# Performance work log

Hardware: AMD Instinct MI355X
Metric: run time of the kernel (lower is better)

## Reference

```python
import jax, jax.numpy as jnp
import numpy as np

B, S, D, H, FF = 2, 4096, 1024, 16, 4096
HD = D // H


def _layernorm(x, g, b, eps=1e-5):
    mu = jnp.mean(x, axis=-1, keepdims=True)
    var = jnp.var(x, axis=-1, keepdims=True)
    return (x - mu) * jax.lax.rsqrt(var + eps) * g + b


def setup_inputs() -> dict:
    key = jax.random.key(0)
    ks = jax.random.split(key, 20)
    sd = 1.0 / np.sqrt(D)
    sf = 1.0 / np.sqrt(FF)
    inp = {
        "x": jax.random.normal(ks[0], (B, S, D), jnp.float32),
        # attention projections, stored as [in, out]
        "wq": jax.random.normal(ks[1], (D, D), jnp.float32) * sd,
        "bq": jnp.zeros((D,), jnp.float32),
        "wk": jax.random.normal(ks[2], (D, D), jnp.float32) * sd,
        "bk": jnp.zeros((D,), jnp.float32),
        "wv": jax.random.normal(ks[3], (D, D), jnp.float32) * sd,
        "bv": jnp.zeros((D,), jnp.float32),
        "wo": jax.random.normal(ks[4], (D, D), jnp.float32) * sd,
        "bo": jnp.zeros((D,), jnp.float32),
        # block norm1 (pre-attention)
        "ln1_g": jnp.ones((D,), jnp.float32),
        "ln1_b": jnp.zeros((D,), jnp.float32),
        # FFN internal norm
        "lnf_g": jnp.ones((D,), jnp.float32),
        "lnf_b": jnp.zeros((D,), jnp.float32),
        # gated FFN
        "w1": jax.random.normal(ks[5], (D, FF), jnp.float32) * sd,
        "b1": jnp.zeros((FF,), jnp.float32),
        "wg": jax.random.normal(ks[6], (D, FF), jnp.float32) * sd,
        "bg": jnp.zeros((FF,), jnp.float32),
        "w2": jax.random.normal(ks[7], (FF, D), jnp.float32) * sf,
        "b2": jnp.zeros((D,), jnp.float32),
    }
    return inp


def reference(x, wq, bq, wk, bk, wv, bv, wo, bo, ln1_g, ln1_b,
              lnf_g, lnf_b, w1, b1, wg, bg, w2, b2):
    # pre-norm attention
    residual = x
    h = _layernorm(x, ln1_g, ln1_b)
    q = (h @ wq + bq).reshape(B, S, H, HD).transpose(0, 2, 1, 3)  # [B,H,S,hd]
    k = (h @ wk + bk).reshape(B, S, H, HD).transpose(0, 2, 1, 3)
    v = (h @ wv + bv).reshape(B, S, H, HD).transpose(0, 2, 1, 3)
    scores = jnp.einsum("bhqd,bhkd->bhqk", q, k) / np.sqrt(HD)
    attn = jax.nn.softmax(scores, axis=-1)  # [B,H,S,S] materialized as in torch src
    ctx = jnp.einsum("bhqk,bhkd->bhqd", attn, v)
    ctx = ctx.transpose(0, 2, 1, 3).reshape(B, S, D)
    attn_out = ctx @ wo + bo
    x = residual + attn_out  # dropout = 0 (eval)

    # gated FFN with internal pre-norm and residual
    res2 = x
    h2 = _layernorm(x, lnf_g, lnf_b)
    gate = jax.nn.sigmoid(h2 @ wg + bg)
    up = jax.nn.gelu(h2 @ w1 + b1, approximate=False)
    out = (up * gate) @ w2 + b2
    return out + res2
```

## Files before the change

kernel.cpp:

```cpp
#include <hip/hip_runtime.h>
#include <hip/hip_bf16.h>

#define BB 2
#define SS 4096
#define DD 1024
#define HH 16
#define HD 64
#define FF 4096
#define MM (BB*SS)
#define QKVW 3072

typedef __hip_bfloat16 bf16;
typedef __attribute__((ext_vector_type(8))) __bf16 v8bf;
typedef __attribute__((ext_vector_type(4))) float f32x4;
typedef __attribute__((ext_vector_type(16))) float f32x16;
typedef __attribute__((ext_vector_type(8))) unsigned short u16v8;

__device__ __forceinline__ f32x4 mfma16(v8bf a, v8bf b, f32x4 c) {
  return __builtin_amdgcn_mfma_f32_16x16x32_bf16(a, b, c, 0, 0, 0);
}
__device__ __forceinline__ f32x16 mfma32(v8bf a, v8bf b, f32x16 c) {
  return __builtin_amdgcn_mfma_f32_32x32x16_bf16(a, b, c, 0, 0, 0);
}
__device__ __forceinline__ void gload16(const void* g, void* l) {
  __builtin_amdgcn_global_load_lds((const __attribute__((address_space(1))) void*)g,
                                   (__attribute__((address_space(3))) void*)l, 16, 0, 0);
}
__device__ __forceinline__ unsigned cvtpk_bf16(float lo, float hi) {
  unsigned r;
  asm("v_cvt_pk_bf16_f32 %0, %1, %2" : "=v"(r) : "v"(lo), "v"(hi));
  return r;
}
__device__ __forceinline__ float fastrcp(float x) {
  float r;
  asm("v_rcp_f32 %0, %1" : "=v"(r) : "v"(x));
  return r;
}

__global__ void k_tcvt(const float* __restrict__ W, bf16* __restrict__ Wt, int K, int N,
                       long rowoff, float scale)
{
  __shared__ float tile[32][33];
  const int n0 = blockIdx.x * 32, k0 = blockIdx.y * 32;
  const int tx = threadIdx.x, ty = threadIdx.y;
#pragma unroll
  for (int i = 0; i < 32; i += 8)
    tile[ty + i][tx] = W[(long)(k0 + ty + i) * N + n0 + tx];
  __syncthreads();
#pragma unroll
  for (int i = 0; i < 32; i += 8)
    Wt[(rowoff + n0 + ty + i) * K + k0 + tx] = __float2bfloat16(tile[tx][ty + i] * scale);
}

__global__ __launch_bounds__(256)
void k_vtrans(const bf16* __restrict__ qkv, bf16* __restrict__ Vt)
{
  __shared__ bf16 tile[64][72];
  const int s0 = blockIdx.x * 64;
  const int h  = blockIdx.y;
  const int b  = blockIdx.z;
  const int t  = threadIdx.x;
  const int r = t >> 3, c8 = t & 7;
#pragma unroll
  for (int it = 0; it < 2; ++it) {
    const int sr = it * 32 + r;
    const u16v8 v =
        *(const u16v8*)(qkv + (long)(b * SS + s0 + sr) * QKVW + 2048 + h * 64 + c8 * 8);
#pragma unroll
    for (int e = 0; e < 8; ++e)
      ((unsigned short*)&tile[sr][0])[c8 * 8 + e] = v[e];
  }
  __syncthreads();
#pragma unroll
  for (int it = 0; it < 2; ++it) {
    const int d = it * 32 + r;
    union { unsigned short s[8]; u16v8 v; } o;
#pragma unroll
    for (int e = 0; e < 8; ++e)
      o.s[e] = ((const unsigned short*)tile)[(c8 * 8 + e) * 72 + d];
    *(u16v8*)(Vt + ((long)(b * HH + h) * HD + d) * (long)SS + s0 + c8 * 8) = o.v;
  }
}

__global__ __launch_bounds__(256)
void k_layernorm(const float* __restrict__ x, const float* __restrict__ g,
                 const float* __restrict__ b, bf16* __restrict__ out)
{
  const int row = blockIdx.x;
  const float4 v = ((const float4*)(x + (long)row * DD))[threadIdx.x];
  float s  = v.x + v.y + v.z + v.w;
  float s2 = v.x*v.x + v.y*v.y + v.z*v.z + v.w*v.w;
#pragma unroll
  for (int off = 1; off < 64; off <<= 1) {
    s  += __shfl_xor(s,  off);
    s2 += __shfl_xor(s2, off);
  }
  __shared__ float red[8];
  if ((threadIdx.x & 63) == 0) {
    red[threadIdx.x >> 6]       = s;
    red[(threadIdx.x >> 6) + 4] = s2;
  }
  __syncthreads();
  s  = red[0] + red[1] + red[2] + red[3];
  s2 = red[4] + red[5] + red[6] + red[7];
  const float mu = s * (1.f / DD);
  const float rs = rsqrtf(s2 * (1.f / DD) - mu * mu + 1e-5f);
  const float4 gv = ((const float4*)g)[threadIdx.x];
  const float4 bv = ((const float4*)b)[threadIdx.x];
  bf16* op = out + (long)row * DD + threadIdx.x * 4;
  op[0] = __float2bfloat16((v.x - mu) * rs * gv.x + bv.x);
  op[1] = __float2bfloat16((v.y - mu) * rs * gv.y + bv.y);
  op[2] = __float2bfloat16((v.z - mu) * rs * gv.z + bv.z);
  op[3] = __float2bfloat16((v.w - mu) * rs * gv.w + bv.w);
}

template<int EPI, int SWZ>
__global__ __launch_bounds__(256, 2)
void k_gemm(const bf16* __restrict__ A, const bf16* __restrict__ Bt,
            const float* __restrict__ bias, const float* __restrict__ bias2,
            const float* __restrict__ bias3, const float* __restrict__ res,
            void* __restrict__ Cout, int M, int N, int K, float scale)
{
  __shared__ __align__(16) bf16 As[128 * 32];
  __shared__ __align__(16) bf16 Bs[128 * 32];
  int bx = blockIdx.x, by = blockIdx.y;
  if (SWZ) {
    const int nwg = gridDim.x * gridDim.y;
    int o = by * gridDim.x + bx;
    o = (o & 7) * (nwg >> 3) + (o >> 3);
    bx = o % gridDim.x;
    by = o / gridDim.x;
  }
  const int t = threadIdx.x;
  const int lane = t & 63, w = t >> 6;
  const int wr = w >> 1, wc = w & 1;
  const int fr = lane & 15, fq = lane >> 4;
  const long m0 = (long)by * 128, n0 = (long)bx * 128;

  f32x4 acc[4][4] = {};

  const bf16* Ag0 = A  + (m0 + (t >> 2)) * K + (t & 3) * 8;
  const bf16* Ag1 = Ag0 + 64L * K;
  const bf16* Bg0 = Bt + (n0 + (t >> 2)) * K + (t & 3) * 8;
  const bf16* Bg1 = Bg0 + 64L * K;

  for (int kk = 0; kk < K; kk += 32) {
    gload16(Ag0 + kk, As + t * 8);
    gload16(Ag1 + kk, As + 2048 + t * 8);
    gload16(Bg0 + kk, Bs + t * 8);
    gload16(Bg1 + kk, Bs + 2048 + t * 8);
    __syncthreads();
    v8bf af[4], bfr[4];
#pragma unroll
    for (int mt = 0; mt < 4; ++mt)
      af[mt] = *(const v8bf*)&As[(wr*64 + mt*16 + fr) * 32 + fq*8];
#pragma unroll
    for (int nt = 0; nt < 4; ++nt)
      bfr[nt] = *(const v8bf*)&Bs[(wc*64 + nt*16 + fr) * 32 + fq*8];
#pragma unroll
    for (int mt = 0; mt < 4; ++mt)
#pragma unroll
      for (int nt = 0; nt < 4; ++nt)
        acc[mt][nt] = mfma16(af[mt], bfr[nt], acc[mt][nt]);
    __syncthreads();
  }

#pragma unroll
  for (int nt = 0; nt < 4; ++nt) {
    const long col = n0 + wc*64 + nt*16 + fr;
    float bv;
    if (EPI == 2) {
      const int seg = (int)(col >> 10);
      bv = (seg == 0) ? bias[col & 1023] * scale
                      : ((seg == 1) ? bias2 : bias3)[col & 1023];
    } else {
      bv = bias[col];
    }
#pragma unroll
    for (int mt = 0; mt < 4; ++mt) {
#pragma unroll
      for (int j = 0; j < 4; ++j) {
        const long row = m0 + wr*64 + mt*16 + fq*4 + j;
        const float v = acc[mt][nt][j] + bv;
        if (EPI == 2) ((bf16*)Cout)[row * N + col] = __float2bfloat16(v);
        else          ((float*)Cout)[row * N + col] = v + res[row * N + col];
      }
    }
  }
}

__global__ __launch_bounds__(256, 2)
void k_ffn_dual(const bf16* __restrict__ A, const bf16* __restrict__ BgT,
                const bf16* __restrict__ BuT, const float* __restrict__ bgb,
                const float* __restrict__ bub, bf16* __restrict__ Out)
{
  __shared__ __align__(16) bf16 As[128 * 32];
  __shared__ __align__(16) bf16 Gs[64 * 32];
  __shared__ __align__(16) bf16 Us[64 * 32];
  const int t = threadIdx.x;
  const int lane = t & 63, w = t >> 6;
  const int wr = w >> 1, wc = w & 1;
  const int fr = lane & 15, fq = lane >> 4;
  const long m0 = (long)blockIdx.y * 128, n0 = (long)blockIdx.x * 64;
  const int K = DD;

  f32x4 ag[4][2] = {}, au[4][2] = {};

  const bf16* Ag0 = A   + (m0 + (t >> 2)) * K + (t & 3) * 8;
  const bf16* Ag1 = Ag0 + 64L * K;
  const bf16* Gg  = BgT + (n0 + (t >> 2)) * K + (t & 3) * 8;
  const bf16* Ug  = BuT + (n0 + (t >> 2)) * K + (t & 3) * 8;

  for (int kk = 0; kk < K; kk += 32) {
    gload16(Ag0 + kk, As + t * 8);
    gload16(Ag1 + kk, As + 2048 + t * 8);
    gload16(Gg + kk, Gs + t * 8);
    gload16(Ug + kk, Us + t * 8);
    __syncthreads();
    v8bf af[4], gf[2], uf[2];
#pragma unroll
    for (int mt = 0; mt < 4; ++mt)
      af[mt] = *(const v8bf*)&As[(wr*64 + mt*16 + fr) * 32 + fq*8];
#pragma unroll
    for (int nt = 0; nt < 2; ++nt) {
      gf[nt] = *(const v8bf*)&Gs[(wc*32 + nt*16 + fr) * 32 + fq*8];
      uf[nt] = *(const v8bf*)&Us[(wc*32 + nt*16 + fr) * 32 + fq*8];
    }
#pragma unroll
    for (int mt = 0; mt < 4; ++mt)
#pragma unroll
      for (int nt = 0; nt < 2; ++nt) {
        ag[mt][nt] = mfma16(af[mt], gf[nt], ag[mt][nt]);
        au[mt][nt] = mfma16(af[mt], uf[nt], au[mt][nt]);
      }
    __syncthreads();
  }

#pragma unroll
  for (int nt = 0; nt < 2; ++nt) {
    const long col = n0 + wc*32 + nt*16 + fr;
    const float gb = bgb[col], ub = bub[col];
#pragma unroll
    for (int mt = 0; mt < 4; ++mt) {
#pragma unroll
      for (int j = 0; j < 4; ++j) {
        const long row = m0 + wr*64 + mt*16 + fq*4 + j;
        const float g = ag[mt][nt][j] + gb;
        const float u = au[mt][nt][j] + ub;
        const float eg = __builtin_amdgcn_exp2f(1.44269504f * g);
        const float sg = eg * fastrcp(1.f + eg);
        const float u3 = u * u * u;
        const float E = __builtin_amdgcn_exp2f(fmaf(0.1029453f, u3, 2.3021858f * u));
        const float gl = u * E * fastrcp(1.f + E);
        Out[row * FF + col] = __float2bfloat16(sg * gl);
      }
    }
  }
}

__global__ __launch_bounds__(256, 2)
void k_attn(const bf16* __restrict__ qkv, const bf16* __restrict__ Vt,
            bf16* __restrict__ ctx)
{
  __shared__ __align__(16) bf16 Ksh[2][4096];
  __shared__ __align__(16) bf16 Vsh[2][4096];
  const int t = threadIdx.x;
  const int lane = t & 63, w = t >> 6;
  const int q5 = lane & 31, hi = lane >> 5;

  int o = blockIdx.x + 32 * (blockIdx.y + 16 * blockIdx.z);
  o = (o & 7) * 128 + (o >> 3);
  const int q0 = (o & 31) * 128;
  const int h = (o >> 5) & 15, b = o >> 9;

  const long qkv_row0 = (long)b * SS * QKVW + h * HD;
  const long ctx_base = (long)b * SS * DD + h * HD;
  const long vt_base  = ((long)(b * HH + h)) * ((long)HD * SS);

  const int r0 = t >> 3;
  const int cswz = ((t & 7) * 16) ^ ((r0 & 7) << 4);
  const bf16* kg = qkv + qkv_row0 + 1024 + (long)r0 * QKVW + (cswz >> 1);
  const bf16* vg = Vt + vt_base + (long)r0 * SS + (cswz >> 1);

  v8bf qf[4];
  {
    const bf16* qp = qkv + qkv_row0 + (long)(q0 + w * 32 + q5) * QKVW + hi * 8;
#pragma unroll
    for (int c = 0; c < 4; ++c) qf[c] = *(const v8bf*)(qp + c * 16);
  }

  int kcol[4];
#pragma unroll
  for (int c = 0; c < 4; ++c)
    kcol[c] = ((c * 32 + hi * 16) ^ ((q5 & 7) << 4)) >> 1;

  float m_ = -1e30f, l_ = 0.f;
  f32x16 o0 = {}, o1 = {};

#define STAGE(bufidx, kv0_) do {                                    \
    const bf16* kp_ = kg + (long)(kv0_) * QKVW;                     \
    gload16(kp_,              &Ksh[bufidx][t * 8]);                 \
    gload16(kp_ + 32L * QKVW, &Ksh[bufidx][2048 + t * 8]);          \
    const bf16* vp_ = vg + (kv0_);                                  \
    gload16(vp_,            &Vsh[bufidx][t * 8]);                   \
    gload16(vp_ + 32L * SS, &Vsh[bufidx][2048 + t * 8]);            \
  } while (0)

  STAGE(0, 0);
  __syncthreads();

  for (int tt = 0; tt < SS / 64; ++tt) {
    const int cur = tt & 1;
    if (tt + 1 < SS / 64) STAGE(cur ^ 1, (tt + 1) * 64);

    f32x16 s0 = {}, s1 = {};
#pragma unroll
    for (int c = 0; c < 4; ++c) {
      const v8bf k0 = *(const v8bf*)&Ksh[cur][q5 * 64 + kcol[c]];
      const v8bf k1 = *(const v8bf*)&Ksh[cur][(32 + q5) * 64 + kcol[c]];
      s0 = mfma32(k0, qf[c], s0);
      s1 = mfma32(k1, qf[c], s1);
    }

    float tm[8];
#pragma unroll
    for (int r = 0; r < 8; ++r)
      tm[r] = fmaxf(fmaxf(s0[r], s0[r + 8]), fmaxf(s1[r], s1[r + 8]));
#pragma unroll
    for (int r = 0; r < 4; ++r) tm[r] = fmaxf(tm[r], tm[r + 4]);
    float pm = fmaxf(fmaxf(tm[0], tm[1]), fmaxf(tm[2], tm[3]));
    pm = fmaxf(pm, __shfl_xor(pm, 32));

    const bool defer = __all(pm - m_ <= 8.f);
    float al = 1.f;
    if (!defer) {
      const float mn = fmaxf(m_, pm);
      al = __builtin_amdgcn_exp2f(m_ - mn);
      m_ = mn;
    }
#pragma unroll
    for (int r = 0; r < 16; ++r) s0[r] = __builtin_amdgcn_exp2f(s0[r] - m_);
#pragma unroll
    for (int r = 0; r < 16; ++r) s1[r] = __builtin_amdgcn_exp2f(s1[r] - m_);
    float a0, a1, a2, a3;
    a0 = s0[0] + s1[0]; a1 = s0[1] + s1[1]; a2 = s0[2] + s1[2]; a3 = s0[3] + s1[3];
#pragma unroll
    for (int r = 4; r < 16; r += 4) {
      a0 += s0[r] + s1[r];
      a1 += s0[r + 1] + s1[r + 1];
      a2 += s0[r + 2] + s1[r + 2];
      a3 += s0[r + 3] + s1[r + 3];
    }
    float rs = (a0 + a1) + (a2 + a3);
    rs += __shfl_xor(rs, 32);
    if (defer) {
      l_ += rs;
    } else {
      l_ = l_ * al + rs;
#pragma unroll
      for (int r = 0; r < 16; ++r) { o0[r] *= al; o1[r] *= al; }
    }

    v8bf pb[4];
#pragma unroll
    for (int c = 0; c < 4; ++c) {
      const int base = (c & 1) * 8;
      unsigned wa0, wa1, wb0, wb1;
      if (c < 2) {
        wa0 = cvtpk_bf16(s0[base + 0], s0[base + 1]);
        wa1 = cvtpk_bf16(s0[base + 2], s0[base + 3]);
        wb0 = cvtpk_bf16(s0[base + 4], s0[base + 5]);
        wb1 = cvtpk_bf16(s0[base + 6], s0[base + 7]);
      } else {
        wa0 = cvtpk_bf16(s1[base + 0], s1[base + 1]);
        wa1 = cvtpk_bf16(s1[base + 2], s1[base + 3]);
        wb0 = cvtpk_bf16(s1[base + 4], s1[base + 5]);
        wb1 = cvtpk_bf16(s1[base + 6], s1[base + 7]);
      }
      asm("v_permlane32_swap_b32 %0, %1" : "+v"(wa0), "+v"(wb0));
      asm("v_permlane32_swap_b32 %0, %1" : "+v"(wa1), "+v"(wb1));
      union { unsigned u[4]; v8bf v; } cvt;
      cvt.u[0] = wa0; cvt.u[1] = wa1; cvt.u[2] = wb0; cvt.u[3] = wb1;
      pb[c] = cvt.v;
    }

#pragma unroll
    for (int c = 0; c < 4; ++c) {
      const v8bf v0f = *(const v8bf*)&Vsh[cur][q5 * 64 + kcol[c]];
      const v8bf v1f = *(const v8bf*)&Vsh[cur][(32 + q5) * 64 + kcol[c]];
      o0 = mfma32(v0f, pb[c], o0);
      o1 = mfma32(v1f, pb[c], o1);
    }
    __syncthreads();
  }
#undef STAGE

  const float inv = 1.f / l_;
  bf16* Osh = &Ksh[0][0];
  const int qrow = w * 32 + q5;
  const int oswz = (qrow & 7) << 4;
#pragma unroll
  for (int r = 0; r < 16; ++r) {
    const int d0 = (r & 3) + 8 * (r >> 2) + 4 * hi;
    Osh[((qrow * 128 + d0 * 2) ^ oswz) >> 1]        = __float2bfloat16(o0[r] * inv);
    Osh[((qrow * 128 + (32 + d0) * 2) ^ oswz) >> 1] = __float2bfloat16(o1[r] * inv);
  }
  __syncthreads();
  {
    const int q = t >> 1, half = t & 1;
    const int qs = (q & 7) << 4;
    bf16* cp = ctx + ctx_base + (long)(q0 + q) * DD + half * 32;
#pragma unroll
    for (int s = 0; s < 4; ++s) {
      const int byte = (q * 128 + half * 64 + s * 16) ^ qs;
      *(u16v8*)(cp + s * 8) = *(const u16v8*)&Osh[byte >> 1];
    }
  }
}

extern "C" void kernel_launch(void* const* d_in, const int* in_sizes, int n_in,
                              void* d_out, int out_size, void* d_ws, size_t ws_size,
                              hipStream_t stream)
{
  const float* x    = (const float*)d_in[0];
  const float* wq   = (const float*)d_in[1];
  const float* bq   = (const float*)d_in[2];
  const float* wk   = (const float*)d_in[3];
  const float* bk   = (const float*)d_in[4];
  const float* wv   = (const float*)d_in[5];
  const float* bv   = (const float*)d_in[6];
  const float* wo   = (const float*)d_in[7];
  const float* bo   = (const float*)d_in[8];
  const float* ln1g = (const float*)d_in[9];
  const float* ln1b = (const float*)d_in[10];
  const float* lnfg = (const float*)d_in[11];
  const float* lnfb = (const float*)d_in[12];
  const float* w1   = (const float*)d_in[13];
  const float* b1   = (const float*)d_in[14];
  const float* wg   = (const float*)d_in[15];
  const float* bg   = (const float*)d_in[16];
  const float* w2   = (const float*)d_in[17];
  const float* b2   = (const float*)d_in[18];

  char* ws = (char*)d_ws;
  const size_t MB = 1u << 20;
  bf16*  WqkvT = (bf16*)(ws + 0 * MB);
  bf16*  WoT   = (bf16*)(ws + 6 * MB);
  bf16*  W1T   = (bf16*)(ws + 8 * MB);
  bf16*  WgT   = (bf16*)(ws + 16 * MB);
  bf16*  W2T   = (bf16*)(ws + 24 * MB);
  float* x1    = (float*)(ws + 32 * MB);
  bf16*  hbuf  = (bf16*)(ws + 64 * MB);
  bf16*  QKVb  = (bf16*)(ws + 80 * MB);
  bf16*  Vtb   = (bf16*)(ws + 128 * MB);
  bf16*  ctxb  = hbuf;
  bf16*  prod  = (bf16*)(ws + 80 * MB);

  const float qscale = 0.1803368801111204f;

  dim3 tb(32, 8);
  k_tcvt<<<dim3(32, 32), tb, 0, stream>>>(wq, WqkvT, 1024, 1024, 0, qscale);
  k_tcvt<<<dim3(32, 32), tb, 0, stream>>>(wk, WqkvT, 1024, 1024, 1024, 1.f);
  k_tcvt<<<dim3(32, 32), tb, 0, stream>>>(wv, WqkvT, 1024, 1024, 2048, 1.f);
  k_tcvt<<<dim3(32, 32), tb, 0, stream>>>(wo, WoT, 1024, 1024, 0, 1.f);
  k_tcvt<<<dim3(128, 32), tb, 0, stream>>>(w1, W1T, 1024, 4096, 0, 1.f);
  k_tcvt<<<dim3(128, 32), tb, 0, stream>>>(wg, WgT, 1024, 4096, 0, 1.f);
  k_tcvt<<<dim3(32, 128), tb, 0, stream>>>(w2, W2T, 4096, 1024, 0, 1.f);

  k_layernorm<<<MM, 256, 0, stream>>>(x, ln1g, ln1b, hbuf);

  k_gemm<2,0><<<dim3(QKVW / 128, MM / 128), 256, 0, stream>>>(
      hbuf, WqkvT, bq, bk, bv, nullptr, QKVb, MM, QKVW, 1024, qscale);

  k_vtrans<<<dim3(SS / 64, HH, BB), 256, 0, stream>>>(QKVb, Vtb);
  k_attn<<<dim3(SS / 128, HH, BB), 256, 0, stream>>>(QKVb, Vtb, ctxb);

  k_gemm<1,0><<<dim3(8, 64), 256, 0, stream>>>(
      ctxb, WoT, bo, nullptr, nullptr, x, x1, MM, 1024, 1024, 1.f);

  k_layernorm<<<MM, 256, 0, stream>>>(x1, lnfg, lnfb, hbuf);

  k_ffn_dual<<<dim3(FF / 64, MM / 128), 256, 0, stream>>>(hbuf, WgT, W1T, bg, b1, prod);

  k_gemm<1,0><<<dim3(8, 64), 256, 0, stream>>>(
      prod, W2T, b2, nullptr, nullptr, x1, (float*)d_out, MM, 1024, 4096, 1.f);
}
```

Before: 597.7 us.

## Load K and V fragments directly from global memory in attention kernel

Removes the double-buffered LDS staging of K and V tiles and the per-iteration block barrier from the flash-attention loop. Each wave now reads its K and V MFMA operands straight from global memory (through L2/L1), and LDS is kept only for the output transpose. This drops the barrier and LDS traffic, but each of the four waves now fetches the same K/V data separately, and without the async prefetch the global-load latency sits on the critical path.

```diff
diff --git a/kernel.cpp b/kernel.cpp
--- a/kernel.cpp
+++ b/kernel.cpp
@@ -262,8 +262,7 @@
 void k_attn(const bf16* __restrict__ qkv, const bf16* __restrict__ Vt,
             bf16* __restrict__ ctx)
 {
-  __shared__ __align__(16) bf16 Ksh[2][4096];
-  __shared__ __align__(16) bf16 Vsh[2][4096];
+  __shared__ __align__(16) bf16 Osh[8192];
   const int t = threadIdx.x;
   const int lane = t & 63, w = t >> 6;
   const int q5 = lane & 31, hi = lane >> 5;
@@ -277,11 +276,6 @@
   const long ctx_base = (long)b * SS * DD + h * HD;
   const long vt_base  = ((long)(b * HH + h)) * ((long)HD * SS);
 
-  const int r0 = t >> 3;
-  const int cswz = ((t & 7) * 16) ^ ((r0 & 7) << 4);
-  const bf16* kg = qkv + qkv_row0 + 1024 + (long)r0 * QKVW + (cswz >> 1);
-  const bf16* vg = Vt + vt_base + (long)r0 * SS + (cswz >> 1);
-
   v8bf qf[4];
   {
     const bf16* qp = qkv + qkv_row0 + (long)(q0 + w * 32 + q5) * QKVW + hi * 8;
@@ -289,37 +283,25 @@
     for (int c = 0; c < 4; ++c) qf[c] = *(const v8bf*)(qp + c * 16);
   }
 
-  int kcol[4];
-#pragma unroll
-  for (int c = 0; c < 4; ++c)
-    kcol[c] = ((c * 32 + hi * 16) ^ ((q5 & 7) << 4)) >> 1;
+  const bf16* kp0 = qkv + qkv_row0 + 1024 + (long)q5 * QKVW + hi * 8;
+  const bf16* vp0 = Vt + vt_base + (long)q5 * SS + hi * 8;
 
   float m_ = -1e30f, l_ = 0.f;
   f32x16 o0 = {}, o1 = {};
 
-#define STAGE(bufidx, kv0_) do {                                    \
-    const bf16* kp_ = kg + (long)(kv0_) * QKVW;                     \
-    gload16(kp_,              &Ksh[bufidx][t * 8]);                 \
-    gload16(kp_ + 32L * QKVW, &Ksh[bufidx][2048 + t * 8]);          \
-    const bf16* vp_ = vg + (kv0_);                                  \
-    gload16(vp_,            &Vsh[bufidx][t * 8]);                   \
-    gload16(vp_ + 32L * SS, &Vsh[bufidx][2048 + t * 8]);            \
-  } while (0)
-
-  STAGE(0, 0);
-  __syncthreads();
-
   for (int tt = 0; tt < SS / 64; ++tt) {
-    const int cur = tt & 1;
-    if (tt + 1 < SS / 64) STAGE(cur ^ 1, (tt + 1) * 64);
+    const long kv0 = (long)tt * 64;
 
     f32x16 s0 = {}, s1 = {};
-#pragma unroll
-    for (int c = 0; c < 4; ++c) {
-      const v8bf k0 = *(const v8bf*)&Ksh[cur][q5 * 64 + kcol[c]];
-      const v8bf k1 = *(const v8bf*)&Ksh[cur][(32 + q5) * 64 + kcol[c]];
-      s0 = mfma32(k0, qf[c], s0);
-      s1 = mfma32(k1, qf[c], s1);
+    {
+      const bf16* kp = kp0 + kv0 * QKVW;
+#pragma unroll
+      for (int c = 0; c < 4; ++c) {
+        const v8bf k0 = *(const v8bf*)(kp + c * 16);
+        const v8bf k1 = *(const v8bf*)(kp + 32L * QKVW + c * 16);
+        s0 = mfma32(k0, qf[c], s0);
+        s1 = mfma32(k1, qf[c], s1);
+      }
     }
 
     float tm[8];
@@ -384,19 +366,19 @@
       pb[c] = cvt.v;
     }
 
-#pragma unroll
-    for (int c = 0; c < 4; ++c) {
-      const v8bf v0f = *(const v8bf*)&Vsh[cur][q5 * 64 + kcol[c]];
-      const v8bf v1f = *(const v8bf*)&Vsh[cur][(32 + q5) * 64 + kcol[c]];
-      o0 = mfma32(v0f, pb[c], o0);
-      o1 = mfma32(v1f, pb[c], o1);
-    }
-    __syncthreads();
-  }
-#undef STAGE
+    {
+      const bf16* vp = vp0 + kv0;
+#pragma unroll
+      for (int c = 0; c < 4; ++c) {
+        const v8bf v0f = *(const v8bf*)(vp + c * 16);
+        const v8bf v1f = *(const v8bf*)(vp + 32L * SS + c * 16);
+        o0 = mfma32(v0f, pb[c], o0);
+        o1 = mfma32(v1f, pb[c], o1);
+      }
+    }
+  }
 
   const float inv = 1.f / l_;
-  bf16* Osh = &Ksh[0][0];
   const int qrow = w * 32 + q5;
   const int oswz = (qrow & 7) << 4;
 #pragma unroll
```

Measured after the change: 869.5 us. +45.5%, slower.

## Split attention KV range in two and merge partial softmax outputs

Applied to the files above, without the earlier changes.

The attention kernel now splits each query tile's key/value sequence into two halves processed by separate blocks, doubling the grid. Each block writes its normalized partial output and its running max and sum. A new combine kernel rescales and merges the two halves into the context buffer. This adds parallelism and occupancy for attention, at the cost of extra global traffic, a second launch, and reuse of the output buffer as scratch for the max/sum statistics.

```diff
diff --git a/kernel.cpp b/kernel.cpp
--- a/kernel.cpp
+++ b/kernel.cpp
@@ -15,6 +15,7 @@
 typedef __attribute__((ext_vector_type(4))) float f32x4;
 typedef __attribute__((ext_vector_type(16))) float f32x16;
 typedef __attribute__((ext_vector_type(8))) unsigned short u16v8;
+typedef __attribute__((ext_vector_type(4))) unsigned short u16v4;
 
 __device__ __forceinline__ f32x4 mfma16(v8bf a, v8bf b, f32x4 c) {
   return __builtin_amdgcn_mfma_f32_16x16x32_bf16(a, b, c, 0, 0, 0);
@@ -35,6 +36,11 @@
   float r;
   asm("v_rcp_f32 %0, %1" : "=v"(r) : "v"(x));
   return r;
+}
+__device__ __forceinline__ float b2f(unsigned short u) {
+  union { unsigned u32; float f; } x;
+  x.u32 = (unsigned)u << 16;
+  return x.f;
 }
 
 __global__ void k_tcvt(const float* __restrict__ W, bf16* __restrict__ Wt, int K, int N,
@@ -260,7 +266,7 @@
 
 __global__ __launch_bounds__(256, 2)
 void k_attn(const bf16* __restrict__ qkv, const bf16* __restrict__ Vt,
-            bf16* __restrict__ ctx)
+            bf16* __restrict__ Osb, float* __restrict__ mlb)
 {
   __shared__ __align__(16) bf16 Ksh[2][4096];
   __shared__ __align__(16) bf16 Vsh[2][4096];
@@ -269,13 +275,15 @@
   const int q5 = lane & 31, hi = lane >> 5;
 
   int o = blockIdx.x + 32 * (blockIdx.y + 16 * blockIdx.z);
-  o = (o & 7) * 128 + (o >> 3);
+  o = (o & 7) * 256 + (o >> 3);
   const int q0 = (o & 31) * 128;
-  const int h = (o >> 5) & 15, b = o >> 9;
+  const int h = (o >> 5) & 15;
+  const int bz = o >> 9;
+  const int b = bz >> 1, sp = bz & 1;
 
   const long qkv_row0 = (long)b * SS * QKVW + h * HD;
-  const long ctx_base = (long)b * SS * DD + h * HD;
   const long vt_base  = ((long)(b * HH + h)) * ((long)HD * SS);
+  const long o_base   = ((long)sp * MM + (long)b * SS) * DD + h * HD;
 
   const int r0 = t >> 3;
   const int cswz = ((t & 7) * 16) ^ ((r0 & 7) << 4);
@@ -306,12 +314,13 @@
     gload16(vp_ + 32L * SS, &Vsh[bufidx][2048 + t * 8]);            \
   } while (0)
 
-  STAGE(0, 0);
+  const int t0 = sp * 32, t1 = t0 + 32;
+  STAGE(0, t0 * 64);
   __syncthreads();
 
-  for (int tt = 0; tt < SS / 64; ++tt) {
+  for (int tt = t0; tt < t1; ++tt) {
     const int cur = tt & 1;
-    if (tt + 1 < SS / 64) STAGE(cur ^ 1, (tt + 1) * 64);
+    if (tt + 1 < t1) STAGE(cur ^ 1, (tt + 1) * 64);
 
     f32x16 s0 = {}, s1 = {};
 #pragma unroll
@@ -395,6 +404,13 @@
   }
 #undef STAGE
 
+  if (hi == 0) {
+    const int row = q0 + w * 32 + q5;
+    const long mi = ((((long)sp * BB + b) * HH + h) * SS + row) * 2;
+    mlb[mi] = m_;
+    mlb[mi + 1] = l_;
+  }
+
   const float inv = 1.f / l_;
   bf16* Osh = &Ksh[0][0];
   const int qrow = w * 32 + q5;
@@ -409,13 +425,45 @@
   {
     const int q = t >> 1, half = t & 1;
     const int qs = (q & 7) << 4;
-    bf16* cp = ctx + ctx_base + (long)(q0 + q) * DD + half * 32;
+    bf16* cp = Osb + o_base + (long)(q0 + q) * DD + half * 32;
 #pragma unroll
     for (int s = 0; s < 4; ++s) {
       const int byte = (q * 128 + half * 64 + s * 16) ^ qs;
       *(u16v8*)(cp + s * 8) = *(const u16v8*)&Osh[byte >> 1];
     }
   }
+}
+
+__global__ __launch_bounds__(256)
+void k_comb(const bf16* __restrict__ Osb, const float* __restrict__ mlb,
+            bf16* __restrict__ ctx)
+{
+  const int row = blockIdx.x;
+  const int b = row >> 12, sr = row & (SS - 1);
+  const int t = threadIdx.x;
+  const int e0 = t * 4;
+  const int h = e0 >> 6;
+  const long i1 = (((long)(0 * BB + b) * HH + h) * SS + sr) * 2;
+  const long i2 = (((long)(1 * BB + b) * HH + h) * SS + sr) * 2;
+  const float m1 = mlb[i1], l1 = mlb[i1 + 1];
+  const float m2 = mlb[i2], l2 = mlb[i2 + 1];
+  const float m = fmaxf(m1, m2);
+  const float W1 = __builtin_amdgcn_exp2f(m1 - m) * l1;
+  const float W2 = __builtin_amdgcn_exp2f(m2 - m) * l2;
+  const float inv = fastrcp(W1 + W2);
+  const float c1 = W1 * inv, c2 = W2 * inv;
+  const long off = (long)row * DD + e0;
+  const u16v4 a = *(const u16v4*)(Osb + off);
+  const u16v4 c = *(const u16v4*)(Osb + (long)MM * DD + off);
+  u16v4 outv;
+#pragma unroll
+  for (int i = 0; i < 4; ++i) {
+    const float v = c1 * b2f(a[i]) + c2 * b2f(c[i]);
+    union { bf16 bh; unsigned short us; } cv;
+    cv.bh = __float2bfloat16(v);
+    outv[i] = cv.us;
+  }
+  *(u16v4*)(ctx + off) = outv;
 }
 
 extern "C" void kernel_launch(void* const* d_in, const int* in_sizes, int n_in,
@@ -450,11 +498,13 @@
   bf16*  WgT   = (bf16*)(ws + 16 * MB);
   bf16*  W2T   = (bf16*)(ws + 24 * MB);
   float* x1    = (float*)(ws + 32 * MB);
+  bf16*  Osb   = (bf16*)(ws + 32 * MB);
   bf16*  hbuf  = (bf16*)(ws + 64 * MB);
   bf16*  QKVb  = (bf16*)(ws + 80 * MB);
   bf16*  Vtb   = (bf16*)(ws + 128 * MB);
   bf16*  ctxb  = hbuf;
   bf16*  prod  = (bf16*)(ws + 80 * MB);
+  float* mlb   = (float*)d_out;
 
   const float qscale = 0.1803368801111204f;
 
@@ -473,7 +523,8 @@
       hbuf, WqkvT, bq, bk, bv, nullptr, QKVb, MM, QKVW, 1024, qscale);
 
   k_vtrans<<<dim3(SS / 64, HH, BB), 256, 0, stream>>>(QKVb, Vtb);
-  k_attn<<<dim3(SS / 128, HH, BB), 256, 0, stream>>>(QKVb, Vtb, ctxb);
+  k_attn<<<dim3(SS / 128, HH, 2 * BB), 256, 0, stream>>>(QKVb, Vtb, Osb, mlb);
+  k_comb<<<MM, 256, 0, stream>>>(Osb, mlb, ctxb);
 
   k_gemm<1,0><<<dim3(8, 64), 256, 0, stream>>>(
       ctxb, WoT, bo, nullptr, nullptr, x, x1, MM, 1024, 1024, 1.f);
```

Result: no change. 607.1 us (+1.6%).

## Double GEMM K-tile to 64 with XOR-swizzled LDS layout

Applied to the files above, without the earlier changes.

Both the generic GEMM and the dual-gate FFN GEMM now stage 64-wide K slices per iteration instead of 32, which halves the number of barrier pairs per K loop. The global-to-LDS copy writes rows with an XOR swizzle on the 16-byte column chunk, and the fragment reads apply the same swizzle, so the wider 128-byte rows do not cause LDS bank conflicts. LDS use per block doubles, which may limit how many blocks fit per CU, and there is still no double buffering.

```diff
diff --git a/kernel.cpp b/kernel.cpp
--- a/kernel.cpp
+++ b/kernel.cpp
@@ -121,8 +121,8 @@
             const float* __restrict__ bias3, const float* __restrict__ res,
             void* __restrict__ Cout, int M, int N, int K, float scale)
 {
-  __shared__ __align__(16) bf16 As[128 * 32];
-  __shared__ __align__(16) bf16 Bs[128 * 32];
+  __shared__ __align__(16) bf16 As[128 * 64];
+  __shared__ __align__(16) bf16 Bs[128 * 64];
   int bx = blockIdx.x, by = blockIdx.y;
   if (SWZ) {
     const int nwg = gridDim.x * gridDim.y;
@@ -139,29 +139,37 @@
 
   f32x4 acc[4][4] = {};
 
-  const bf16* Ag0 = A  + (m0 + (t >> 2)) * K + (t & 3) * 8;
-  const bf16* Ag1 = Ag0 + 64L * K;
-  const bf16* Bg0 = Bt + (n0 + (t >> 2)) * K + (t & 3) * 8;
-  const bf16* Bg1 = Bg0 + 64L * K;
-
-  for (int kk = 0; kk < K; kk += 32) {
-    gload16(Ag0 + kk, As + t * 8);
-    gload16(Ag1 + kk, As + 2048 + t * 8);
-    gload16(Bg0 + kk, Bs + t * 8);
-    gload16(Bg1 + kk, Bs + 2048 + t * 8);
+  const int r0 = t >> 3;
+  const int cswz = ((t & 7) * 16) ^ ((r0 & 7) << 4);
+  const bf16* Ag = A  + (m0 + r0) * K + (cswz >> 1);
+  const bf16* Bg = Bt + (n0 + r0) * K + (cswz >> 1);
+
+  for (int kk = 0; kk < K; kk += 64) {
+#pragma unroll
+    for (int ch = 0; ch < 4; ++ch) {
+      gload16(Ag + (long)ch * 32 * K + kk, As + ch * 2048 + t * 8);
+      gload16(Bg + (long)ch * 32 * K + kk, Bs + ch * 2048 + t * 8);
+    }
     __syncthreads();
-    v8bf af[4], bfr[4];
-#pragma unroll
-    for (int mt = 0; mt < 4; ++mt)
-      af[mt] = *(const v8bf*)&As[(wr*64 + mt*16 + fr) * 32 + fq*8];
-#pragma unroll
-    for (int nt = 0; nt < 4; ++nt)
-      bfr[nt] = *(const v8bf*)&Bs[(wc*64 + nt*16 + fr) * 32 + fq*8];
-#pragma unroll
-    for (int mt = 0; mt < 4; ++mt)
-#pragma unroll
-      for (int nt = 0; nt < 4; ++nt)
-        acc[mt][nt] = mfma16(af[mt], bfr[nt], acc[mt][nt]);
+#pragma unroll
+    for (int ks = 0; ks < 2; ++ks) {
+      v8bf af[4], bfr[4];
+#pragma unroll
+      for (int mt = 0; mt < 4; ++mt) {
+        const int rr = wr*64 + mt*16 + fr;
+        af[mt] = *(const v8bf*)&As[rr*64 + (((ks*64 + fq*16) ^ ((rr & 7) << 4)) >> 1)];
+      }
+#pragma unroll
+      for (int nt = 0; nt < 4; ++nt) {
+        const int rr = wc*64 + nt*16 + fr;
+        bfr[nt] = *(const v8bf*)&Bs[rr*64 + (((ks*64 + fq*16) ^ ((rr & 7) << 4)) >> 1)];
+      }
+#pragma unroll
+      for (int mt = 0; mt < 4; ++mt)
+#pragma unroll
+        for (int nt = 0; nt < 4; ++nt)
+          acc[mt][nt] = mfma16(af[mt], bfr[nt], acc[mt][nt]);
+    }
     __syncthreads();
   }
 
@@ -194,9 +202,9 @@
                 const bf16* __restrict__ BuT, const float* __restrict__ bgb,
                 const float* __restrict__ bub, bf16* __restrict__ Out)
 {
-  __shared__ __align__(16) bf16 As[128 * 32];
-  __shared__ __align__(16) bf16 Gs[64 * 32];
-  __shared__ __align__(16) bf16 Us[64 * 32];
+  __shared__ __align__(16) bf16 As[128 * 64];
+  __shared__ __align__(16) bf16 Gs[64 * 64];
+  __shared__ __align__(16) bf16 Us[64 * 64];
   const int t = threadIdx.x;
   const int lane = t & 63, w = t >> 6;
   const int wr = w >> 1, wc = w & 1;
@@ -206,33 +214,45 @@
 
   f32x4 ag[4][2] = {}, au[4][2] = {};
 
-  const bf16* Ag0 = A   + (m0 + (t >> 2)) * K + (t & 3) * 8;
-  const bf16* Ag1 = Ag0 + 64L * K;
-  const bf16* Gg  = BgT + (n0 + (t >> 2)) * K + (t & 3) * 8;
-  const bf16* Ug  = BuT + (n0 + (t >> 2)) * K + (t & 3) * 8;
-
-  for (int kk = 0; kk < K; kk += 32) {
-    gload16(Ag0 + kk, As + t * 8);
-    gload16(Ag1 + kk, As + 2048 + t * 8);
-    gload16(Gg + kk, Gs + t * 8);
-    gload16(Ug + kk, Us + t * 8);
+  const int r0 = t >> 3;
+  const int cswz = ((t & 7) * 16) ^ ((r0 & 7) << 4);
+  const bf16* Ag = A   + (m0 + r0) * K + (cswz >> 1);
+  const bf16* Gg = BgT + (n0 + r0) * K + (cswz >> 1);
+  const bf16* Ug = BuT + (n0 + r0) * K + (cswz >> 1);
+
+  for (int kk = 0; kk < K; kk += 64) {
+#pragma unroll
+    for (int ch = 0; ch < 4; ++ch)
+      gload16(Ag + (long)ch * 32 * K + kk, As + ch * 2048 + t * 8);
+#pragma unroll
+    for (int ch = 0; ch < 2; ++ch) {
+      gload16(Gg + (long)ch * 32 * K + kk, Gs + ch * 2048 + t * 8);
+      gload16(Ug + (long)ch * 32 * K + kk, Us + ch * 2048 + t * 8);
+    }
     __syncthreads();
-    v8bf af[4], gf[2], uf[2];
-#pragma unroll
-    for (int mt = 0; mt < 4; ++mt)
-      af[mt] = *(const v8bf*)&As[(wr*64 + mt*16 + fr) * 32 + fq*8];
-#pragma unroll
-    for (int nt = 0; nt < 2; ++nt) {
-      gf[nt] = *(const v8bf*)&Gs[(wc*32 + nt*16 + fr) * 32 + fq*8];
-      uf[nt] = *(const v8bf*)&Us[(wc*32 + nt*16 + fr) * 32 + fq*8];
-    }
-#pragma unroll
-    for (int mt = 0; mt < 4; ++mt)
+#pragma unroll
+    for (int ks = 0; ks < 2; ++ks) {
+      v8bf af[4], gf[2], uf[2];
+#pragma unroll
+      for (int mt = 0; mt < 4; ++mt) {
+        const int rr = wr*64 + mt*16 + fr;
+        af[mt] = *(const v8bf*)&As[rr*64 + (((ks*64 + fq*16) ^ ((rr & 7) << 4)) >> 1)];
+      }
 #pragma unroll
       for (int nt = 0; nt < 2; ++nt) {
-        ag[mt][nt] = mfma16(af[mt], gf[nt], ag[mt][nt]);
-        au[mt][nt] = mfma16(af[mt], uf[nt], au[mt][nt]);
-      }
+        const int rr = wc*32 + nt*16 + fr;
+        const int ce = (((ks*64 + fq*16) ^ ((rr & 7) << 4)) >> 1);
+        gf[nt] = *(const v8bf*)&Gs[rr*64 + ce];
+        uf[nt] = *(const v8bf*)&Us[rr*64 + ce];
+      }
+#pragma unroll
+      for (int mt = 0; mt < 4; ++mt)
+#pragma unroll
+        for (int nt = 0; nt < 2; ++nt) {
+          ag[mt][nt] = mfma16(af[mt], gf[nt], ag[mt][nt]);
+          au[mt][nt] = mfma16(af[mt], uf[nt], au[mt][nt]);
+        }
+    }
     __syncthreads();
   }
 
```

Result: faster. 559.3 us, median of 2 (-6.4%).
